# Kernel tuning notes

Hardware: AMD Instinct MI355X
Metric: run time of the kernel (lower is better)

## Reference

```python
import jax, jax.numpy as jnp
import numpy as np

B, N, D, H = 8, 1024, 768, 12
Dh = D // H


def setup_inputs() -> dict:
    key = jax.random.key(0)
    ks = jax.random.split(key, 9)
    s = 1.0 / np.sqrt(D)
    return {
        "x": jax.random.normal(ks[0], (B, N, D), dtype=jnp.float32),
        "Wq": jax.random.normal(ks[1], (D, D), dtype=jnp.float32) * s,
        "bq": jax.random.normal(ks[2], (D,), dtype=jnp.float32) * 0.01,
        "Wk": jax.random.normal(ks[3], (D, D), dtype=jnp.float32) * s,
        "bk": jax.random.normal(ks[4], (D,), dtype=jnp.float32) * 0.01,
        "Wv": jax.random.normal(ks[5], (D, D), dtype=jnp.float32) * s,
        "bv": jax.random.normal(ks[6], (D,), dtype=jnp.float32) * 0.01,
        "Wo": jax.random.normal(ks[7], (D, D), dtype=jnp.float32) * s,
        "bo": jax.random.normal(ks[8], (D,), dtype=jnp.float32) * 0.01,
    }


def _split_heads(t):
    # [B, N, D] -> [B, H, N, Dh]   ('b n (h d) -> b h n d')
    b, n, d = t.shape
    return t.reshape(b, n, H, Dh).transpose(0, 2, 1, 3)


def reference(x, Wq, bq, Wk, bk, Wv, bv, Wo, bo):
    q = _split_heads(x @ Wq.T + bq)
    k = _split_heads(x @ Wk.T + bk)
    v = _split_heads(x @ Wv.T + bv)
    scale = 1.0 / jnp.sqrt(jnp.asarray(Dh, dtype=x.dtype))
    scores = jnp.einsum('bhnd,bhmd->bhnm', q, k) * scale  # [B,H,N,N]
    # Faithful to source: F.softmax(..., dim=1) normalizes over the HEAD axis.
    attn = jax.nn.softmax(scores, axis=1)
    out = jnp.einsum('bhnm,bhmd->bhnd', attn, v)          # [B,H,N,Dh]
    out = out.transpose(0, 2, 1, 3).reshape(x.shape)      # 'b h n d -> b n (h d)'
    return out @ Wo.T + bo
```

## Files before the change

### kernel.cpp

```cpp
#include <hip/hip_runtime.h>
#include <hip/hip_bf16.h>

typedef unsigned short u16;
typedef unsigned long long u64;
typedef __bf16 bfv8 __attribute__((ext_vector_type(8)));
typedef float fv4 __attribute__((ext_vector_type(4)));

static __device__ __forceinline__ u16 f2bf(float f) {
    unsigned u = __builtin_bit_cast(unsigned, f);
    unsigned r = (u + 0x7fffu + ((u >> 16) & 1u)) >> 16;
    return (u16)r;
}

static __device__ __forceinline__ void gld16(const void* g, void* l) {
    __builtin_amdgcn_global_load_lds(
        (const __attribute__((address_space(1))) void*)g,
        (__attribute__((address_space(3))) void*)l, 16, 0, 0);
}

__global__ __launch_bounds__(256) void cvt_f32_bf16(
    const float* __restrict__ x, const float* __restrict__ wq,
    const float* __restrict__ wk, const float* __restrict__ wv,
    const float* __restrict__ wo, u16* __restrict__ dst)
{
    int i = blockIdx.x * 256 + threadIdx.x;
    const int NX4 = 6291456 / 4;
    const int NW4 = 589824 / 4;
    const float4* src;
    int j = i;
    if (j < NX4) { src = (const float4*)x; }
    else {
        j -= NX4;
        if (j < NW4) { src = (const float4*)wq; }
        else {
            j -= NW4;
            if (j < NW4) { src = (const float4*)wk; }
            else {
                j -= NW4;
                if (j < NW4) { src = (const float4*)wv; }
                else { j -= NW4; src = (const float4*)wo; }
            }
        }
    }
    float4 v = src[j];
    u64 pk = (u64)f2bf(v.x) | ((u64)f2bf(v.y) << 16) |
             ((u64)f2bf(v.z) << 32) | ((u64)f2bf(v.w) << 48);
    *(u64*)(dst + (size_t)i * 4) = pk;
}

__global__ __launch_bounds__(256) void gemm_bt(
    const u16* __restrict__ A, const u16* __restrict__ Bw,
    const float* __restrict__ bias, u16* __restrict__ Cb,
    float* __restrict__ Cf, int mode)
{
    __shared__ alignas(16) u16 lA[128 * 32];
    __shared__ alignas(16) u16 lB[128 * 32];
    const int t = threadIdx.x;
    const int w = t >> 6, l = t & 63;
    const int l15 = l & 15, l4 = l >> 4;
    const int bx = blockIdx.x, by = blockIdx.y;
    const int wr = (w >> 1) * 64, wc = (w & 1) * 64;
    const int srow = t >> 2;
    const int sg = t & 3;

    fv4 acc[4][4] = {};

    for (int kt = 0; kt < 24; ++kt) {
        const int kof = kt * 32;
        #pragma unroll
        for (int is = 0; is < 2; ++is) {
            int row = is * 64 + srow;
            int gs = sg ^ ((row >> 1) & 3);
            gld16(A + (size_t)(bx * 128 + row) * 768 + kof + gs * 8,
                  &lA[row * 32 + sg * 8]);
            gld16(Bw + (size_t)(by * 128 + row) * 768 + kof + gs * 8,
                  &lB[row * 32 + sg * 8]);
        }
        __syncthreads();

        bfv8 aF[4], bF[4];
        #pragma unroll
        for (int f = 0; f < 4; ++f) {
            int ra = wr + f * 16 + l15;
            aF[f] = *(const bfv8*)&lA[ra * 32 + (l4 ^ ((ra >> 1) & 3)) * 8];
            int rb = wc + f * 16 + l15;
            bF[f] = *(const bfv8*)&lB[rb * 32 + (l4 ^ ((rb >> 1) & 3)) * 8];
        }
        #pragma unroll
        for (int fm = 0; fm < 4; ++fm)
            #pragma unroll
            for (int fn = 0; fn < 4; ++fn)
                acc[fm][fn] = __builtin_amdgcn_mfma_f32_16x16x32_bf16(
                    aF[fm], bF[fn], acc[fm][fn], 0, 0, 0);
        __syncthreads();
    }

    #pragma unroll
    for (int fm = 0; fm < 4; ++fm) {
        #pragma unroll
        for (int fn = 0; fn < 4; ++fn) {
            int n = by * 128 + wc + fn * 16 + l15;
            float bs = bias[n];
            #pragma unroll
            for (int rr = 0; rr < 4; ++rr) {
                int m = bx * 128 + wr + fm * 16 + l4 * 4 + rr;
                float v = acc[fm][fn][rr] + bs;
                if (mode == 2) {
                    Cf[(size_t)m * 768 + n] = v;
                } else {
                    int b = m >> 10, tok = m & 1023;
                    int h = n >> 6, dl = n & 63;
                    size_t addr = (mode == 0)
                        ? (((size_t)(b * 12 + h) * 1024 + tok) * 64 + dl)
                        : (((size_t)(b * 12 + h) * 64 + dl) * 1024 + tok);
                    Cb[addr] = f2bf(v);
                }
            }
        }
    }
}

__global__ __launch_bounds__(256, 1) void scores_smax(
    const u16* __restrict__ qb, const u16* __restrict__ kb,
    u16* __restrict__ attn, int b0)
{
    __shared__ alignas(16) u16 lK[2 * 12 * 32 * 64];
    const int t = threadIdx.x;
    const int w = t >> 6, l = t & 63;
    const int l15 = l & 15, l4 = l >> 4;
    const int bl = blockIdx.y;
    const int b = b0 + bl;
    const int nsub = w & 1, mh = w >> 1;
    const int nbase = blockIdx.x * 32 + nsub * 16;

    bfv8 Qf[12][2];
    #pragma unroll
    for (int h = 0; h < 12; ++h)
        #pragma unroll
        for (int ks = 0; ks < 2; ++ks)
            Qf[h][ks] = *(const bfv8*)(qb +
                ((size_t)(b * 12 + h) * 1024 + nbase + l15) * 64 + ks * 32 + l4 * 8);

    const int sml = t >> 3;
    const int sgp = t & 7;
    const int sgs = sgp ^ (sml & 7);

    for (int mt = 0; mt < 16; ++mt) {
        #pragma unroll
        for (int p = 0; p < 2; ++p)
            #pragma unroll
            for (int h = 0; h < 12; ++h)
                gld16(kb + ((size_t)(b * 12 + h) * 1024 + p * 512 + mt * 32 + sml) * 64 + sgs * 8,
                      &lK[p * 24576 + h * 2048 + sml * 64 + sgp * 8]);
        __syncthreads();

        fv4 S[12][2];
        #pragma unroll
        for (int h = 0; h < 12; ++h) {
            #pragma unroll
            for (int mf = 0; mf < 2; ++mf) {
                fv4 s = {};
                #pragma unroll
                for (int ks = 0; ks < 2; ++ks) {
                    int ml = mf * 16 + l15;
                    int gd = ks * 4 + l4;
                    bfv8 kf = *(const bfv8*)&lK[mh * 24576 + h * 2048 + ml * 64 +
                                                (gd ^ (ml & 7)) * 8];
                    s = __builtin_amdgcn_mfma_f32_16x16x32_bf16(kf, Qf[h][ks], s, 0, 0, 0);
                }
                S[h][mf] = s;
            }
        }

        #pragma unroll
        for (int mf = 0; mf < 2; ++mf) {
            #pragma unroll
            for (int rr = 0; rr < 4; ++rr) {
                float mx = S[0][mf][rr];
                #pragma unroll
                for (int h = 1; h < 12; ++h) mx = fmaxf(mx, S[h][mf][rr]);
                float pp[12];
                float sum = 0.f;
                #pragma unroll
                for (int h = 0; h < 12; ++h) {
                    pp[h] = __builtin_amdgcn_exp2f((S[h][mf][rr] - mx) *
                                                   (0.125f * 1.44269504f));
                    sum += pp[h];
                }
                float r = __builtin_amdgcn_rcpf(sum);
                #pragma unroll
                for (int h = 0; h < 12; ++h) S[h][mf][rr] = pp[h] * r;
            }
        }

        #pragma unroll
        for (int h = 0; h < 12; ++h) {
            #pragma unroll
            for (int mf = 0; mf < 2; ++mf) {
                u64 pk = (u64)f2bf(S[h][mf][0]) | ((u64)f2bf(S[h][mf][1]) << 16) |
                         ((u64)f2bf(S[h][mf][2]) << 32) | ((u64)f2bf(S[h][mf][3]) << 48);
                size_t m = (size_t)mh * 512 + mt * 32 + mf * 16 + l4 * 4;
                *(u64*)(attn + ((size_t)(bl * 12 + h) * 1024 + nbase + l15) * 1024 + m) = pk;
            }
        }
        __syncthreads();
    }
}

__global__ __launch_bounds__(256) void pv_gemm(
    const u16* __restrict__ attn, const u16* __restrict__ vtb,
    u16* __restrict__ ctx, int b0)
{
    __shared__ alignas(16) u16 lA[64 * 64];
    __shared__ alignas(16) u16 lV[64 * 64];
    const int t = threadIdx.x, w = t >> 6, l = t & 63;
    const int l15 = l & 15, l4 = l >> 4;
    const int bx = blockIdx.x, h = blockIdx.y, bl = blockIdx.z;
    const int b = b0 + bl;
    const int srow0 = t >> 3, sgp = t & 7;
    const int sgs = sgp ^ (srow0 & 7);

    fv4 acc[4] = {};
    const size_t abase = ((size_t)(bl * 12 + h) * 1024 + bx * 64) * 1024;
    const size_t vbase = (size_t)(b * 12 + h) * 64 * 1024;

    for (int mt = 0; mt < 16; ++mt) {
        #pragma unroll
        for (int is = 0; is < 2; ++is) {
            int row = is * 32 + srow0;
            gld16(attn + abase + (size_t)row * 1024 + mt * 64 + sgs * 8,
                  &lA[row * 64 + sgp * 8]);
            gld16(vtb + vbase + (size_t)row * 1024 + mt * 64 + sgs * 8,
                  &lV[row * 64 + sgp * 8]);
        }
        __syncthreads();

        #pragma unroll
        for (int ks = 0; ks < 2; ++ks) {
            int ra = w * 16 + l15;
            int gd = ks * 4 + l4;
            bfv8 aF = *(const bfv8*)&lA[ra * 64 + (gd ^ (ra & 7)) * 8];
            #pragma unroll
            for (int dn = 0; dn < 4; ++dn) {
                int rv = dn * 16 + l15;
                bfv8 vF = *(const bfv8*)&lV[rv * 64 + (gd ^ (rv & 7)) * 8];
                acc[dn] = __builtin_amdgcn_mfma_f32_16x16x32_bf16(aF, vF, acc[dn], 0, 0, 0);
            }
        }
        __syncthreads();
    }

    #pragma unroll
    for (int dn = 0; dn < 4; ++dn) {
        #pragma unroll
        for (int rr = 0; rr < 4; ++rr) {
            int tok = bx * 64 + w * 16 + l4 * 4 + rr;
            int dl = dn * 16 + l15;
            ctx[((size_t)b * 1024 + tok) * 768 + h * 64 + dl] = f2bf(acc[dn][rr]);
        }
    }
}

extern "C" void kernel_launch(void* const* d_in, const int* in_sizes, int n_in,
                              void* d_out, int out_size, void* d_ws, size_t ws_size,
                              hipStream_t stream)
{
    const float* x  = (const float*)d_in[0];
    const float* Wq = (const float*)d_in[1];
    const float* bq = (const float*)d_in[2];
    const float* Wk = (const float*)d_in[3];
    const float* bk = (const float*)d_in[4];
    const float* Wv = (const float*)d_in[5];
    const float* bv = (const float*)d_in[6];
    const float* Wo = (const float*)d_in[7];
    const float* bo = (const float*)d_in[8];
    float* out = (float*)d_out;

    u16* ws  = (u16*)d_ws;
    u16* xb  = ws;
    u16* wqb = xb + 6291456;
    u16* wkb = wqb + 589824;
    u16* wvb = wkb + 589824;
    u16* wob = wvb + 589824;
    u16* qb  = wob + 589824;
    u16* kbuf= qb + 6291456;
    u16* vtb = kbuf + 6291456;
    u16* ctx = vtb + 6291456;
    u16* attnb = ctx + 6291456;

    const size_t FIXED_BYTES = (size_t)(attnb - ws) * 2;
    size_t avail = ws_size > FIXED_BYTES ? ws_size - FIXED_BYTES : 0;
    int nb = 8;
    while (nb > 1 && (size_t)nb * 25165824ull > avail) nb >>= 1;
    int nchunks = 8 / nb;

    cvt_f32_bf16<<<dim3(8448), dim3(256), 0, stream>>>(x, Wq, Wk, Wv, Wo, ws);

    gemm_bt<<<dim3(64, 6), dim3(256), 0, stream>>>(xb, wqb, bq, qb, nullptr, 0);
    gemm_bt<<<dim3(64, 6), dim3(256), 0, stream>>>(xb, wkb, bk, kbuf, nullptr, 0);
    gemm_bt<<<dim3(64, 6), dim3(256), 0, stream>>>(xb, wvb, bv, vtb, nullptr, 1);

    for (int c = 0; c < nchunks; ++c) {
        scores_smax<<<dim3(32, nb), dim3(256), 0, stream>>>(qb, kbuf, attnb, c * nb);
        pv_gemm<<<dim3(16, 12, nb), dim3(256), 0, stream>>>(attnb, vtb, ctx, c * nb);
    }

    gemm_bt<<<dim3(64, 6), dim3(256), 0, stream>>>(ctx, wob, bo, nullptr, out, 2);
}
```

Measured before the change: 436.1 us.

## Fuse head-axis softmax with PV into one attention kernel, drop attn buffer

Replaces the separate scores+softmax kernel and PV GEMM with a single fused kernel that computes scores per head, normalizes across heads in registers, and immediately multiplies by V. The large bf16 attention matrix no longer goes through global memory. The softmax scale and log2e are folded into the Q projection epilogue. The max subtraction is dropped, and Q/K are stored token-major and read directly from global memory without LDS staging. Risks include the lower occupancy of 128-thread blocks holding large register arrays, uncoalesced direct K/V loads, and possible overflow of exp2 without the max subtraction.

```diff
diff --git a/kernel.cpp b/kernel.cpp
--- a/kernel.cpp
+++ b/kernel.cpp
@@ -2,14 +2,22 @@
 #include <hip/hip_bf16.h>
 
 typedef unsigned short u16;
+typedef unsigned int   u32;
 typedef unsigned long long u64;
 typedef __bf16 bfv8 __attribute__((ext_vector_type(8)));
-typedef float fv4 __attribute__((ext_vector_type(4)));
+typedef float  fv4  __attribute__((ext_vector_type(4)));
+typedef u32    uv4  __attribute__((ext_vector_type(4)));
 
 static __device__ __forceinline__ u16 f2bf(float f) {
     unsigned u = __builtin_bit_cast(unsigned, f);
     unsigned r = (u + 0x7fffu + ((u >> 16) & 1u)) >> 16;
     return (u16)r;
+}
+
+static __device__ __forceinline__ u32 cvtpk(float a, float b) {
+    u32 r;
+    asm("v_cvt_pk_bf16_f32 %0, %1, %2" : "=v"(r) : "v"(a), "v"(b));
+    return r;
 }
 
 static __device__ __forceinline__ void gld16(const void* g, void* l) {
@@ -51,7 +59,7 @@
 __global__ __launch_bounds__(256) void gemm_bt(
     const u16* __restrict__ A, const u16* __restrict__ Bw,
     const float* __restrict__ bias, u16* __restrict__ Cb,
-    float* __restrict__ Cf, int mode)
+    float* __restrict__ Cf, float scale, int mode)
 {
     __shared__ alignas(16) u16 lA[128 * 32];
     __shared__ alignas(16) u16 lB[128 * 32];
@@ -104,159 +112,120 @@
             #pragma unroll
             for (int rr = 0; rr < 4; ++rr) {
                 int m = bx * 128 + wr + fm * 16 + l4 * 4 + rr;
-                float v = acc[fm][fn][rr] + bs;
+                float v = (acc[fm][fn][rr] + bs) * scale;
                 if (mode == 2) {
                     Cf[(size_t)m * 768 + n] = v;
+                } else if (mode == 3) {
+                    Cb[(size_t)m * 768 + n] = f2bf(v);
                 } else {
                     int b = m >> 10, tok = m & 1023;
                     int h = n >> 6, dl = n & 63;
-                    size_t addr = (mode == 0)
-                        ? (((size_t)(b * 12 + h) * 1024 + tok) * 64 + dl)
-                        : (((size_t)(b * 12 + h) * 64 + dl) * 1024 + tok);
-                    Cb[addr] = f2bf(v);
+                    Cb[((size_t)(b * 12 + h) * 64 + dl) * 1024 + tok] = f2bf(v);
                 }
             }
         }
     }
 }
 
-__global__ __launch_bounds__(256, 1) void scores_smax(
+__global__ __launch_bounds__(128, 1) void fused_attn(
     const u16* __restrict__ qb, const u16* __restrict__ kb,
-    u16* __restrict__ attn, int b0)
-{
-    __shared__ alignas(16) u16 lK[2 * 12 * 32 * 64];
+    const u16* __restrict__ vtb, u16* __restrict__ ctx)
+{
+    __shared__ fv4 red[12 * 4 * 64];
     const int t = threadIdx.x;
-    const int w = t >> 6, l = t & 63;
-    const int l15 = l & 15, l4 = l >> 4;
-    const int bl = blockIdx.y;
-    const int b = b0 + bl;
-    const int nsub = w & 1, mh = w >> 1;
-    const int nbase = blockIdx.x * 32 + nsub * 16;
+    const int mh = t >> 6;
+    const int l = t & 63, l15 = l & 15, l4 = l >> 4;
+    const int b = blockIdx.y;
+    const int nbase = blockIdx.x * 16;
 
     bfv8 Qf[12][2];
+    const u16* qrow = qb + (size_t)(b * 1024 + nbase + l15) * 768;
     #pragma unroll
     for (int h = 0; h < 12; ++h)
         #pragma unroll
         for (int ks = 0; ks < 2; ++ks)
-            Qf[h][ks] = *(const bfv8*)(qb +
-                ((size_t)(b * 12 + h) * 1024 + nbase + l15) * 64 + ks * 32 + l4 * 8);
-
-    const int sml = t >> 3;
-    const int sgp = t & 7;
-    const int sgs = sgp ^ (sml & 7);
+            Qf[h][ks] = *(const bfv8*)(qrow + h * 64 + ks * 32 + l4 * 8);
+
+    fv4 acc[12][4] = {};
 
     for (int mt = 0; mt < 16; ++mt) {
-        #pragma unroll
-        for (int p = 0; p < 2; ++p)
-            #pragma unroll
-            for (int h = 0; h < 12; ++h)
-                gld16(kb + ((size_t)(b * 12 + h) * 1024 + p * 512 + mt * 32 + sml) * 64 + sgs * 8,
-                      &lK[p * 24576 + h * 2048 + sml * 64 + sgp * 8]);
-        __syncthreads();
-
-        fv4 S[12][2];
+        const int mbase = mh * 512 + mt * 32;
+
+        fv4 E[12][2];
+        fv4 dsum[2] = {};
         #pragma unroll
         for (int h = 0; h < 12; ++h) {
             #pragma unroll
             for (int mf = 0; mf < 2; ++mf) {
+                const u16* krow = kb +
+                    (size_t)(b * 1024 + mbase + mf * 16 + l15) * 768 + h * 64;
                 fv4 s = {};
                 #pragma unroll
                 for (int ks = 0; ks < 2; ++ks) {
-                    int ml = mf * 16 + l15;
-                    int gd = ks * 4 + l4;
-                    bfv8 kf = *(const bfv8*)&lK[mh * 24576 + h * 2048 + ml * 64 +
-                                                (gd ^ (ml & 7)) * 8];
-                    s = __builtin_amdgcn_mfma_f32_16x16x32_bf16(kf, Qf[h][ks], s, 0, 0, 0);
+                    bfv8 kf = *(const bfv8*)(krow + ks * 32 + l4 * 8);
+                    s = __builtin_amdgcn_mfma_f32_16x16x32_bf16(
+                            kf, Qf[h][ks], s, 0, 0, 0);
                 }
-                S[h][mf] = s;
-            }
-        }
-
-        #pragma unroll
-        for (int mf = 0; mf < 2; ++mf) {
-            #pragma unroll
-            for (int rr = 0; rr < 4; ++rr) {
-                float mx = S[0][mf][rr];
+                fv4 e;
                 #pragma unroll
-                for (int h = 1; h < 12; ++h) mx = fmaxf(mx, S[h][mf][rr]);
-                float pp[12];
-                float sum = 0.f;
+                for (int rr = 0; rr < 4; ++rr)
+                    e[rr] = __builtin_amdgcn_exp2f(s[rr]);
+                dsum[mf] += e;
+                E[h][mf] = e;
+            }
+        }
+
+        fv4 rs[2];
+        #pragma unroll
+        for (int mf = 0; mf < 2; ++mf)
+            #pragma unroll
+            for (int rr = 0; rr < 4; ++rr)
+                rs[mf][rr] = __builtin_amdgcn_rcpf(dsum[mf][rr]);
+
+        #pragma unroll
+        for (int h = 0; h < 12; ++h) {
+            uv4 tp;
+            tp[0] = cvtpk(E[h][0][0] * rs[0][0], E[h][0][1] * rs[0][1]);
+            tp[1] = cvtpk(E[h][0][2] * rs[0][2], E[h][0][3] * rs[0][3]);
+            tp[2] = cvtpk(E[h][1][0] * rs[1][0], E[h][1][1] * rs[1][1]);
+            tp[3] = cvtpk(E[h][1][2] * rs[1][2], E[h][1][3] * rs[1][3]);
+            bfv8 pa = __builtin_bit_cast(bfv8, tp);
+
+            const u16* vbh = vtb + ((size_t)(b * 12 + h) * 64 + l15) * 1024
+                             + mbase + l4 * 4;
+            #pragma unroll
+            for (int dn = 0; dn < 4; ++dn) {
+                const u16* vp = vbh + (size_t)dn * 16 * 1024;
+                uint2 lo = *(const uint2*)(vp);
+                uint2 hi = *(const uint2*)(vp + 16);
+                uv4 tv; tv[0] = lo.x; tv[1] = lo.y; tv[2] = hi.x; tv[3] = hi.y;
+                bfv8 vf = __builtin_bit_cast(bfv8, tv);
+                acc[h][dn] = __builtin_amdgcn_mfma_f32_16x16x32_bf16(
+                                 pa, vf, acc[h][dn], 0, 0, 0);
+            }
+        }
+    }
+
+    #pragma unroll
+    for (int h = 0; h < 12; ++h) {
+        if ((h / 6) != mh) {
+            #pragma unroll
+            for (int dn = 0; dn < 4; ++dn)
+                red[(h * 4 + dn) * 64 + l] = acc[h][dn];
+        }
+    }
+    __syncthreads();
+    #pragma unroll
+    for (int h = 0; h < 12; ++h) {
+        if ((h / 6) == mh) {
+            #pragma unroll
+            for (int dn = 0; dn < 4; ++dn) {
+                fv4 o = acc[h][dn] + red[(h * 4 + dn) * 64 + l];
                 #pragma unroll
-                for (int h = 0; h < 12; ++h) {
-                    pp[h] = __builtin_amdgcn_exp2f((S[h][mf][rr] - mx) *
-                                                   (0.125f * 1.44269504f));
-                    sum += pp[h];
-                }
-                float r = __builtin_amdgcn_rcpf(sum);
-                #pragma unroll
-                for (int h = 0; h < 12; ++h) S[h][mf][rr] = pp[h] * r;
-            }
-        }
-
-        #pragma unroll
-        for (int h = 0; h < 12; ++h) {
-            #pragma unroll
-            for (int mf = 0; mf < 2; ++mf) {
-                u64 pk = (u64)f2bf(S[h][mf][0]) | ((u64)f2bf(S[h][mf][1]) << 16) |
-                         ((u64)f2bf(S[h][mf][2]) << 32) | ((u64)f2bf(S[h][mf][3]) << 48);
-                size_t m = (size_t)mh * 512 + mt * 32 + mf * 16 + l4 * 4;
-                *(u64*)(attn + ((size_t)(bl * 12 + h) * 1024 + nbase + l15) * 1024 + m) = pk;
-            }
-        }
-        __syncthreads();
-    }
-}
-
-__global__ __launch_bounds__(256) void pv_gemm(
-    const u16* __restrict__ attn, const u16* __restrict__ vtb,
-    u16* __restrict__ ctx, int b0)
-{
-    __shared__ alignas(16) u16 lA[64 * 64];
-    __shared__ alignas(16) u16 lV[64 * 64];
-    const int t = threadIdx.x, w = t >> 6, l = t & 63;
-    const int l15 = l & 15, l4 = l >> 4;
-    const int bx = blockIdx.x, h = blockIdx.y, bl = blockIdx.z;
-    const int b = b0 + bl;
-    const int srow0 = t >> 3, sgp = t & 7;
-    const int sgs = sgp ^ (srow0 & 7);
-
-    fv4 acc[4] = {};
-    const size_t abase = ((size_t)(bl * 12 + h) * 1024 + bx * 64) * 1024;
-    const size_t vbase = (size_t)(b * 12 + h) * 64 * 1024;
-
-    for (int mt = 0; mt < 16; ++mt) {
-        #pragma unroll
-        for (int is = 0; is < 2; ++is) {
-            int row = is * 32 + srow0;
-            gld16(attn + abase + (size_t)row * 1024 + mt * 64 + sgs * 8,
-                  &lA[row * 64 + sgp * 8]);
-            gld16(vtb + vbase + (size_t)row * 1024 + mt * 64 + sgs * 8,
-                  &lV[row * 64 + sgp * 8]);
-        }
-        __syncthreads();
-
-        #pragma unroll
-        for (int ks = 0; ks < 2; ++ks) {
-            int ra = w * 16 + l15;
-            int gd = ks * 4 + l4;
-            bfv8 aF = *(const bfv8*)&lA[ra * 64 + (gd ^ (ra & 7)) * 8];
-            #pragma unroll
-            for (int dn = 0; dn < 4; ++dn) {
-                int rv = dn * 16 + l15;
-                bfv8 vF = *(const bfv8*)&lV[rv * 64 + (gd ^ (rv & 7)) * 8];
-                acc[dn] = __builtin_amdgcn_mfma_f32_16x16x32_bf16(aF, vF, acc[dn], 0, 0, 0);
-            }
-        }
-        __syncthreads();
-    }
-
-    #pragma unroll
-    for (int dn = 0; dn < 4; ++dn) {
-        #pragma unroll
-        for (int rr = 0; rr < 4; ++rr) {
-            int tok = bx * 64 + w * 16 + l4 * 4 + rr;
-            int dl = dn * 16 + l15;
-            ctx[((size_t)b * 1024 + tok) * 768 + h * 64 + dl] = f2bf(acc[dn][rr]);
+                for (int rr = 0; rr < 4; ++rr)
+                    ctx[(size_t)(b * 1024 + nbase + l4 * 4 + rr) * 768 +
+                        h * 64 + dn * 16 + l15] = f2bf(o[rr]);
+            }
         }
     }
 }
@@ -286,24 +255,16 @@
     u16* kbuf= qb + 6291456;
     u16* vtb = kbuf + 6291456;
     u16* ctx = vtb + 6291456;
-    u16* attnb = ctx + 6291456;
-
-    const size_t FIXED_BYTES = (size_t)(attnb - ws) * 2;
-    size_t avail = ws_size > FIXED_BYTES ? ws_size - FIXED_BYTES : 0;
-    int nb = 8;
-    while (nb > 1 && (size_t)nb * 25165824ull > avail) nb >>= 1;
-    int nchunks = 8 / nb;
+
+    const float qscale = 0.125f * 1.44269504089f;
 
     cvt_f32_bf16<<<dim3(8448), dim3(256), 0, stream>>>(x, Wq, Wk, Wv, Wo, ws);
 
-    gemm_bt<<<dim3(64, 6), dim3(256), 0, stream>>>(xb, wqb, bq, qb, nullptr, 0);
-    gemm_bt<<<dim3(64, 6), dim3(256), 0, stream>>>(xb, wkb, bk, kbuf, nullptr, 0);
-    gemm_bt<<<dim3(64, 6), dim3(256), 0, stream>>>(xb, wvb, bv, vtb, nullptr, 1);
-
-    for (int c = 0; c < nchunks; ++c) {
-        scores_smax<<<dim3(32, nb), dim3(256), 0, stream>>>(qb, kbuf, attnb, c * nb);
-        pv_gemm<<<dim3(16, 12, nb), dim3(256), 0, stream>>>(attnb, vtb, ctx, c * nb);
-    }
-
-    gemm_bt<<<dim3(64, 6), dim3(256), 0, stream>>>(ctx, wob, bo, nullptr, out, 2);
-}
+    gemm_bt<<<dim3(64, 6), dim3(256), 0, stream>>>(xb, wqb, bq, qb,  nullptr, qscale, 3);
+    gemm_bt<<<dim3(64, 6), dim3(256), 0, stream>>>(xb, wkb, bk, kbuf, nullptr, 1.0f,  3);
+    gemm_bt<<<dim3(64, 6), dim3(256), 0, stream>>>(xb, wvb, bv, vtb, nullptr, 1.0f,  1);
+
+    fused_attn<<<dim3(64, 8), dim3(128), 0, stream>>>(qb, kbuf, vtb, ctx);
+
+    gemm_bt<<<dim3(64, 6), dim3(256), 0, stream>>>(ctx, wob, bo, nullptr, out, 1.0f, 2);
+}
```

Measured after the change: 591.1 us. +35.6%, slower.
